# Kernel tuning notes

Measured on AMD Instinct MI355X. Metric: run time of the kernel, lower is better.

The kernel has to match this reference:

```python
import jax, jax.numpy as jnp
import numpy as np

N, B, H, L, FE = 32768, 256, 128, 4, 4
E = 262144


def setup_inputs() -> dict:
    key = jax.random.key(0)
    ks = jax.random.split(key, 16)
    def g(i, shape, scale=0.05):
        return jax.random.normal(ks[i], shape, dtype=jnp.float32) * scale
    return {
        "d": jax.random.uniform(ks[0], (E,), dtype=jnp.float32) * 5.0,
        "src": jax.random.randint(ks[1], (E,), 0, N),
        "dst": jax.random.randint(ks[2], (E,), 0, N),
        "seg": jnp.sort(jax.random.randint(ks[3], (N,), 0, B)),
        "node_emb": g(4, (H,), 1.0),
        "We": g(5, (2 * FE + 1, H)), "be": jnp.zeros((H,), jnp.float32),
        "msg_W1": g(6, (L, 3 * H, H)), "msg_b1": jnp.zeros((L, H), jnp.float32),
        "msg_W2": g(7, (L, H, H)), "msg_b2": jnp.zeros((L, H), jnp.float32),
        "soft_W": g(8, (L, H)), "soft_b": jnp.zeros((L,), jnp.float32),
        "upd_W1": g(9, (L, H, H)), "upd_b1": jnp.zeros((L, H), jnp.float32),
        "upd_W2": g(10, (L, H, H)), "upd_b2": jnp.zeros((L, H), jnp.float32),
        "out_W1": g(11, (H, H)), "out_b1": jnp.zeros((H,), jnp.float32),
        "out_W2": g(12, (H, H)), "out_b2": jnp.zeros((H,), jnp.float32),
    }


def reference(d, src, dst, seg, node_emb, We, be, msg_W1, msg_b1, msg_W2, msg_b2,
              soft_W, soft_b, upd_W1, upd_b1, upd_W2, upd_b2,
              out_W1, out_b1, out_W2, out_b2):
    silu = jax.nn.silu
    # fourier_encode_dist: [E] -> [E, 2*FE+1] = [sin(d/2^k), cos(d/2^k), d]
    scales = 2.0 ** jnp.arange(FE, dtype=d.dtype)
    x = d[:, None] / scales
    de = jnp.concatenate([jnp.sin(x), jnp.cos(x), d[:, None]], axis=-1)
    # edge_input MLP (1 layer, last_activation=SiLU) then extra F.silu in input_edge_func
    e = silu(silu(de @ We + be))                              # [E, H]
    # node_embedding broadcast to all nodes
    feat = jnp.broadcast_to(node_emb, (N, H))
    for l in range(L):
        mi = jnp.concatenate([feat[src], feat[dst], e], axis=-1)        # [E, 3H]
        m = silu(silu(mi @ msg_W1[l] + msg_b1[l]) @ msg_W2[l] + msg_b2[l])  # [E, H]
        e = e + m                                             # edge residual update
        w = jax.nn.sigmoid(m @ soft_W[l] + soft_b[l])[:, None]  # soft edge gate [E,1]
        msum = jax.ops.segment_sum(m * w, dst, num_segments=N)  # reduce to dst nodes
        upd_in = msum + feat
        feat = silu(upd_in @ upd_W1[l] + upd_b1[l]) @ upd_W2[l] + upd_b2[l] + feat
    # node-wise output network (2 layers, last activation None)
    feat = silu(feat @ out_W1 + out_b1) @ out_W2 + out_b2
    # multi-aggregator readout over graphs in batch
    s = jax.ops.segment_sum(feat, seg, num_segments=B)
    cnt = jax.ops.segment_sum(jnp.ones((N, 1), feat.dtype), seg, num_segments=B)
    mean = s / jnp.maximum(cnt, 1.0)
    mx = jax.ops.segment_max(feat, seg, num_segments=B)
    return jnp.concatenate([s, mean, mx], axis=-1)            # [B, 3H]
```

## Files before the change

kernel.cpp:

```cpp
#include <hip/hip_runtime.h>

#define NN 32768
#define NB 256
#define HD 128
#define NL 4
#define NE 262144

typedef short bf16x8 __attribute__((ext_vector_type(8)));
typedef float f32x4 __attribute__((ext_vector_type(4)));
typedef unsigned short u16;
typedef unsigned int u32;

__device__ __forceinline__ float bf2f(u16 u) {
  return __uint_as_float(((u32)u) << 16);
}
__device__ __forceinline__ u16 f2bf(float f) {
  u32 x = __float_as_uint(f);
  u32 r = x + 0x7FFFu + ((x >> 16) & 1u);
  return (u16)(r >> 16);
}
__device__ __forceinline__ u32 pk2(float a, float b) {
  return (u32)f2bf(a) | ((u32)f2bf(b) << 16);
}
__device__ __forceinline__ float siluf(float x) {
  return x * __builtin_amdgcn_rcpf(1.0f + __expf(-x));
}
__device__ __forceinline__ float sigf(float x) {
  return __builtin_amdgcn_rcpf(1.0f + __expf(-x));
}
__device__ __forceinline__ u32 ordu(float f) {
  u32 b = __float_as_uint(f);
  return (b & 0x80000000u) ? ~b : (b | 0x80000000u);
}

__device__ __forceinline__ float ldinf(const void* p, size_t i, int mode) {
  return mode ? ((const float*)p)[i] : bf2f(((const u16*)p)[i]);
}
__device__ __forceinline__ u16 ldinb(const void* p, size_t i, int mode) {
  return mode ? f2bf(((const float*)p)[i]) : ((const u16*)p)[i];
}

__global__ void k_detect(const u16* __restrict__ Weraw, int* __restrict__ flag) {
  if (threadIdx.x == 0 && blockIdx.x == 0) {
    int cnt = 0;
    for (int i = 0; i < 256; i++) {
      u16 u = Weraw[2 * i];
      u32 e = (u >> 7) & 0xFFu;
      if (e >= 112u && e <= 126u) cnt++;
    }
    *flag = (cnt >= 128) ? 0 : 1;
  }
}

__global__ __launch_bounds__(256) void k_csr_deg(const int* __restrict__ dstp,
                                                 u32* __restrict__ deg) {
  const int i = blockIdx.x * 256 + threadIdx.x;
  atomicAdd(&deg[dstp[i]], 1u);
}

__global__ __launch_bounds__(1024) void k_csr_scan(const u32* __restrict__ deg,
                                                   int* __restrict__ rowptr,
                                                   int* __restrict__ cursor) {
  __shared__ int part[1024];
  const int t = threadIdx.x;
  int loc[32];
  int s = 0;
#pragma unroll
  for (int j = 0; j < 32; j++) { loc[j] = s; s += (int)deg[t * 32 + j]; }
  part[t] = s;
  __syncthreads();
  int inc = s;
  for (int off = 1; off < 1024; off <<= 1) {
    int tmp = (t >= off) ? part[t - off] : 0;
    __syncthreads();
    part[t] += tmp;
    __syncthreads();
  }
  const int base = part[t] - inc;
#pragma unroll
  for (int j = 0; j < 32; j++) {
    rowptr[t * 32 + j] = base + loc[j];
    cursor[t * 32 + j] = base + loc[j];
  }
  if (t == 1023) rowptr[NN] = part[1023];
}

__global__ __launch_bounds__(256) void k_csr_scatter(const int* __restrict__ dstp,
                                                     int* __restrict__ cursor,
                                                     int* __restrict__ eids) {
  const int i = blockIdx.x * 256 + threadIdx.x;
  const int pos = atomicAdd(&cursor[dstp[i]], 1);
  eids[pos] = i;
}

#define PANEL 16384

template <int MT>
__device__ __forceinline__ void acc_zero(f32x4 (&acc)[MT][8]) {
#pragma unroll
  for (int mt = 0; mt < MT; mt++)
#pragma unroll
    for (int nt = 0; nt < 8; nt++) acc[mt][nt] = f32x4{0.f, 0.f, 0.f, 0.f};
}

template <int MT>
__device__ __forceinline__ void gemm_gp(const u16* __restrict__ A0,
                                        const size_t* rowoff,
                                        const u16* __restrict__ Bp,
                                        int l, int kg, f32x4 (&acc)[MT][8]) {
#pragma unroll
  for (int ks = 0; ks < 4; ks++) {
    bf16x8 a[MT];
#pragma unroll
    for (int mt = 0; mt < MT; mt++)
      a[mt] = *(const bf16x8*)&A0[rowoff[mt] + ks * 32 + kg * 8];
#pragma unroll
    for (int nt = 0; nt < 8; nt++) {
      bf16x8 b = *(const bf16x8*)&Bp[(size_t)((nt * 4 + ks) * 64 + l) * 8];
#pragma unroll
      for (int mt = 0; mt < MT; mt++)
        acc[mt][nt] = __builtin_amdgcn_mfma_f32_16x16x32_bf16(a[mt], b, acc[mt][nt], 0, 0, 0);
    }
  }
}

template <int MT>
__device__ __forceinline__ void wave_gemm_p(const short* lAw, const u16* __restrict__ Bp,
                                            int l, int c, int kg, f32x4 (&acc)[MT][8]) {
#pragma unroll
  for (int ks = 0; ks < 4; ks++) {
    bf16x8 a[MT];
#pragma unroll
    for (int mt = 0; mt < MT; mt++) {
      const int r = mt * 16 + c;
      const int k = ks * 32 + kg * 8;
      a[mt] = *(const bf16x8*)&lAw[r * HD + (k ^ ((r & 7) << 3))];
    }
#pragma unroll
    for (int nt = 0; nt < 8; nt++) {
      bf16x8 b = *(const bf16x8*)&Bp[(size_t)((nt * 4 + ks) * 64 + l) * 8];
#pragma unroll
      for (int mt = 0; mt < MT; mt++)
        acc[mt][nt] = __builtin_amdgcn_mfma_f32_16x16x32_bf16(a[mt], b, acc[mt][nt], 0, 0, 0);
    }
  }
}

template <int MT, bool SILU>
__device__ __forceinline__ void wave_pack(short* lAw, int c, int kg,
                                          f32x4 (&acc)[MT][8], const float* bias) {
#pragma unroll
  for (int mt = 0; mt < MT; mt++) {
#pragma unroll
    for (int rr = 0; rr < 4; rr++) {
      const int row = mt * 16 + kg * 4 + rr;
      u32 ou[4];
#pragma unroll
      for (int p = 0; p < 4; p++) {
        float x0 = acc[mt][2 * p][rr] + bias[2 * p];
        float x1 = acc[mt][2 * p + 1][rr] + bias[2 * p + 1];
        if (SILU) { x0 = siluf(x0); x1 = siluf(x1); }
        ou[p] = pk2(x0, x1);
      }
      ((int4*)(lAw + row * HD))[c ^ (row & 7)] =
          make_int4((int)ou[0], (int)ou[1], (int)ou[2], (int)ou[3]);
    }
  }
}

__global__ __launch_bounds__(256) void k_prep(
    const void* __restrict__ mW1, const void* __restrict__ mW2,
    const void* __restrict__ uW1, const void* __restrict__ uW2,
    const void* __restrict__ oW1, const void* __restrict__ oW2,
    const int* __restrict__ flagp,
    u16* __restrict__ Wt1, u16* __restrict__ Wt2p,
    u16* __restrict__ Wtu1, u16* __restrict__ Wtu2p,
    u16* __restrict__ Wto1, u16* __restrict__ Wto2p) {
  const int mode = *flagp;
  const int tid = blockIdx.x * blockDim.x + threadIdx.x;
  const int stride = gridDim.x * blockDim.x;
  for (int i = tid; i < NL * 3 * PANEL; i += stride) {
    const int l = i / (3 * PANEL), r = i % (3 * PANEL);
    const int chunk = r / PANEL, r2 = r % PANEL;
    const int nt = r2 / 2048, ks = (r2 % 2048) / 512;
    const int lane = (r2 % 512) / 8, j = r2 % 8;
    const int k = chunk * 128 + ks * 32 + (lane >> 4) * 8 + j;
    const int n = nt * 16 + (lane & 15);
    Wt1[i] = ldinb(mW1, ((size_t)l * 384 + k) * HD + n, mode);
  }
  for (int i = tid; i < NL * PANEL; i += stride) {
    const int l = i / PANEL, r = i % PANEL;
    const int nt = r / 2048, ks = (r % 2048) / 512;
    const int lane = (r % 512) / 8, j = r % 8;
    const int k = ks * 32 + (lane >> 4) * 8 + j;
    const int n = nt * 16 + (lane & 15);
    const int hp = ((k & 7) << 4) | (k >> 3);
    Wt2p[i] = ldinb(mW2, ((size_t)l * HD + hp) * HD + n, mode);
    Wtu1[i] = ldinb(uW1, ((size_t)l * HD + k) * HD + n, mode);
    Wtu2p[i] = ldinb(uW2, ((size_t)l * HD + hp) * HD + n, mode);
  }
  for (int i = tid; i < PANEL; i += stride) {
    const int nt = i / 2048, ks = (i % 2048) / 512;
    const int lane = (i % 512) / 8, j = i % 8;
    const int k = ks * 32 + (lane >> 4) * 8 + j;
    const int n = nt * 16 + (lane & 15);
    const int hp = ((k & 7) << 4) | (k >> 3);
    Wto1[i] = ldinb(oW1, (size_t)k * HD + n, mode);
    Wto2p[i] = ldinb(oW2, (size_t)hp * HD + n, mode);
  }
}

__global__ __launch_bounds__(256) void k_featinit(const void* __restrict__ nemb,
                                                  const int* __restrict__ flagp,
                                                  u16* __restrict__ feat) {
  const int mode = *flagp;
  const int i = blockIdx.x * 256 + threadIdx.x;
  const int g = i & 15;
  u32 ou[4];
#pragma unroll
  for (int p = 0; p < 4; p++) {
    u16 a = ldinb(nemb, g * 8 + 2 * p, mode);
    u16 b = ldinb(nemb, g * 8 + 2 * p + 1, mode);
    ou[p] = (u32)a | ((u32)b << 16);
  }
  ((int4*)feat)[i] = make_int4((int)ou[0], (int)ou[1], (int)ou[2], (int)ou[3]);
}

__global__ __launch_bounds__(256) void k_encode(const void* __restrict__ d,
                                                const void* __restrict__ We,
                                                const void* __restrict__ be,
                                                const int* __restrict__ flagp,
                                                u16* __restrict__ e) {
  const int mode = *flagp;
  __shared__ float sW[9 * HD];
  __shared__ float sb[HD];
  for (int i = threadIdx.x; i < 9 * HD; i += 256) sW[i] = ldinf(We, i, mode);
  for (int i = threadIdx.x; i < HD; i += 256) sb[i] = ldinf(be, i, mode);
  __syncthreads();
  const int eid = blockIdx.x * 256 + threadIdx.x;
  const float dv = ldinf(d, eid, mode);
  float de[9];
#pragma unroll
  for (int k = 0; k < 4; k++) {
    float x = dv * (1.0f / (float)(1 << k));
    de[k] = __sinf(x);
    de[4 + k] = __cosf(x);
  }
  de[8] = dv;
  u16* erow = e + (size_t)eid * HD;
#pragma unroll
  for (int hb = 0; hb < 16; hb++) {
    u32 ou[4];
#pragma unroll
    for (int p = 0; p < 4; p++) {
      float vv[2];
#pragma unroll
      for (int t = 0; t < 2; t++) {
        const int h = hb * 8 + 2 * p + t;
        float a = sb[h];
#pragma unroll
        for (int k = 0; k < 9; k++) a += de[k] * sW[k * HD + h];
        vv[t] = siluf(siluf(a));
      }
      ou[p] = pk2(vv[0], vv[1]);
    }
    ((int4*)erow)[hb] = make_int4((int)ou[0], (int)ou[1], (int)ou[2], (int)ou[3]);
  }
}

__global__ __launch_bounds__(64, 4) void k_edge(
    const u16* __restrict__ feat, u16* __restrict__ e,
    const int* __restrict__ src, const int* __restrict__ dstp,
    const u16* __restrict__ Wt1, const u16* __restrict__ Wt2p,
    const void* __restrict__ b1g, const void* __restrict__ b2g,
    const void* __restrict__ softW, const void* __restrict__ softb,
    const int* __restrict__ flagp, u32* __restrict__ mbuf32,
    float* __restrict__ wgbuf, int layer) {
  __shared__ __align__(16) short lM[32 * HD];
  __shared__ float swg[32];
  const int mode = *flagp;
  const int l = threadIdx.x;
  const int c = l & 15, kg = l >> 4;
  const int blk = blockIdx.x * 32;

  size_t offS[2], offD[2], offE[2];
#pragma unroll
  for (int mt = 0; mt < 2; mt++) {
    const int eidx = blk + mt * 16 + c;
    offS[mt] = (size_t)src[eidx] * HD;
    offD[mt] = (size_t)dstp[eidx] * HD;
    offE[mt] = (size_t)eidx * HD;
  }

  const u16* W1l = Wt1 + (size_t)layer * 3 * PANEL;
  const u16* W2l = Wt2p + (size_t)layer * PANEL;
  float bias1[8], bias2[8], swf[8];
#pragma unroll
  for (int nt = 0; nt < 8; nt++) {
    bias1[nt] = ldinf(b1g, layer * HD + nt * 16 + c, mode);
    bias2[nt] = ldinf(b2g, layer * HD + nt * 16 + c, mode);
    swf[nt] = ldinf(softW, (size_t)layer * HD + nt * 16 + c, mode);
  }
  const float sbv = ldinf(softb, layer, mode);

  f32x4 acc[2][8];
  acc_zero<2>(acc);
  gemm_gp<2>(feat, offS, W1l, l, kg, acc);
  gemm_gp<2>(feat, offD, W1l + PANEL, l, kg, acc);
  gemm_gp<2>(e, offE, W1l + 2 * PANEL, l, kg, acc);
  wave_pack<2, true>(lM, c, kg, acc, bias1);
  __syncthreads();

  acc_zero<2>(acc);
  wave_gemm_p<2>(lM, W2l, l, c, kg, acc);
  __syncthreads();

  float wred[2][4];
#pragma unroll
  for (int mt = 0; mt < 2; mt++) {
#pragma unroll
    for (int rr = 0; rr < 4; rr++) {
      const int row = mt * 16 + kg * 4 + rr;
      float mv[8];
      float wp = 0.f;
#pragma unroll
      for (int nt = 0; nt < 8; nt++) {
        mv[nt] = siluf(acc[mt][nt][rr] + bias2[nt]);
        wp += mv[nt] * swf[nt];
      }
      u32 ou[4];
#pragma unroll
      for (int p = 0; p < 4; p++) ou[p] = pk2(mv[2 * p], mv[2 * p + 1]);
      ((int4*)(lM + row * HD))[c ^ (row & 7)] =
          make_int4((int)ou[0], (int)ou[1], (int)ou[2], (int)ou[3]);
      wp += __shfl_xor(wp, 1);
      wp += __shfl_xor(wp, 2);
      wp += __shfl_xor(wp, 4);
      wp += __shfl_xor(wp, 8);
      wred[mt][rr] = wp;
    }
  }
#pragma unroll
  for (int mt = 0; mt < 2; mt++)
#pragma unroll
    for (int rr = 0; rr < 4; rr++)
      if (c == mt * 4 + rr) swg[mt * 16 + kg * 4 + rr] = sigf(wred[mt][rr] + sbv);
  __syncthreads();

  if (l < 32) wgbuf[blk + l] = swg[l];

  const int j1 = l >> 4;
  const int goff = l & 15;
  const bool hilane = (l >= 32);
  const int s0 = (2 * l) & 63, s1 = (2 * l + 1) & 63;
#pragma unroll 4
  for (int r = 0; r < 32; r++) {
    const int base = r * HD + ((goff ^ (r & 7)) << 3) + j1;
    const u32 m1 = (u16)lM[base];
    const u32 m2 = (u16)lM[base + 4];
    const u32 pk = m1 | (m2 << 16);
    const u32 a = (u32)__shfl((int)pk, s0);
    const u32 b = (u32)__shfl((int)pk, s1);
    const u32 lo = hilane ? (a >> 16) : (a & 0xffffu);
    const u32 hi = hilane ? (b >> 16) : (b & 0xffffu);
    mbuf32[(size_t)(blk + r) * 64 + l] = lo | (hi << 16);
    u32* erow32 = (u32*)(e + (size_t)(blk + r) * HD);
    const u32 old = erow32[l];
    erow32[l] = pk2(bf2f((u16)(old & 0xffffu)) + bf2f((u16)lo),
                    bf2f((u16)(old >> 16)) + bf2f((u16)hi));
  }
}

__global__ __launch_bounds__(256) void k_gather(
    const int* __restrict__ rowptr, const int* __restrict__ eids,
    const u32* __restrict__ mbuf32, const float* __restrict__ wgbuf,
    float* __restrict__ msum) {
  const int w = threadIdx.x >> 6;
  const int l = threadIdx.x & 63;
  const int node = blockIdx.x * 4 + w;
  const int beg = rowptr[node], end = rowptr[node + 1];
  float a0 = 0.f, a1 = 0.f;
  for (int cb = beg; cb < end; cb += 64) {
    int eL = 0;
    float wL = 0.f;
    if (cb + l < end) { eL = eids[cb + l]; wL = wgbuf[eL]; }
    const int nj = min(64, end - cb);
    for (int j = 0; j < nj; j++) {
      const int eid = __shfl(eL, j);
      const float wj = __shfl(wL, j);
      const u32 v = mbuf32[(size_t)eid * 64 + l];
      a0 += wj * bf2f((u16)(v & 0xffffu));
      a1 += wj * bf2f((u16)(v >> 16));
    }
  }
  ((float2*)(msum + (size_t)node * HD))[l] = make_float2(a0, a1);
}

__global__ __launch_bounds__(64, 2) void k_node(
    u16* __restrict__ feat, const float* __restrict__ msum,
    const u16* __restrict__ Wtu1, const u16* __restrict__ Wtu2p,
    const void* __restrict__ b1g, const void* __restrict__ b2g,
    const int* __restrict__ flagp, int layer) {
  __shared__ __align__(16) short lA[64 * HD];
  const int mode = *flagp;
  const int l = threadIdx.x;
  const int c = l & 15, kg = l >> 4;
  short* lAw = lA;
  const int blkn = blockIdx.x * 64;
  const int myrow = blkn + l;
  u16* frow = feat + (size_t)myrow * HD;
  const float* mrow = msum + (size_t)myrow * HD;
  const u16* W1l = Wtu1 + (size_t)layer * PANEL;
  const u16* W2l = Wtu2p + (size_t)layer * PANEL;
  float bias1[8], bias2[8];
#pragma unroll
  for (int nt = 0; nt < 8; nt++) {
    bias1[nt] = ldinf(b1g, layer * HD + nt * 16 + c, mode);
    bias2[nt] = ldinf(b2g, layer * HD + nt * 16 + c, mode);
  }
  {
    int4* lrow = (int4*)(lAw + l * HD);
#pragma unroll
    for (int g = 0; g < 16; g++) {
      int4 fv = ((const int4*)frow)[g];
      u32 uu[4] = {(u32)fv.x, (u32)fv.y, (u32)fv.z, (u32)fv.w};
      float4 ma = ((const float4*)mrow)[2 * g];
      float4 mb = ((const float4*)mrow)[2 * g + 1];
      float mm[8] = {ma.x, ma.y, ma.z, ma.w, mb.x, mb.y, mb.z, mb.w};
      u32 ou[4];
#pragma unroll
      for (int p = 0; p < 4; p++) {
        float a0 = bf2f((u16)(uu[p] & 0xffffu)) + mm[2 * p];
        float a1 = bf2f((u16)(uu[p] >> 16)) + mm[2 * p + 1];
        ou[p] = pk2(a0, a1);
      }
      lrow[g ^ (l & 7)] = make_int4((int)ou[0], (int)ou[1], (int)ou[2], (int)ou[3]);
    }
  }
  __syncthreads();
  f32x4 acc[4][8];
  acc_zero<4>(acc);
  wave_gemm_p<4>(lAw, W1l, l, c, kg, acc);
  __syncthreads();
  wave_pack<4, true>(lAw, c, kg, acc, bias1);
  __syncthreads();
  acc_zero<4>(acc);
  wave_gemm_p<4>(lAw, W2l, l, c, kg, acc);
  __syncthreads();
  wave_pack<4, false>(lAw, c, kg, acc, bias2);
  __syncthreads();

  const int j1 = l >> 4;
  const int goff = l & 15;
  const bool hilane = (l >= 32);
  const int s0 = (2 * l) & 63, s1 = (2 * l + 1) & 63;
#pragma unroll 4
  for (int r = 0; r < 64; r++) {
    const int base = r * HD + ((goff ^ (r & 7)) << 3) + j1;
    const u32 m1 = (u16)lAw[base];
    const u32 m2 = (u16)lAw[base + 4];
    const u32 pk = m1 | (m2 << 16);
    const u32 a = (u32)__shfl((int)pk, s0);
    const u32 b = (u32)__shfl((int)pk, s1);
    const u32 lo = hilane ? (a >> 16) : (a & 0xffffu);
    const u32 hi = hilane ? (b >> 16) : (b & 0xffffu);
    u32* frow32 = (u32*)(feat + (size_t)(blkn + r) * HD);
    const u32 old = frow32[l];
    frow32[l] = pk2(bf2f((u16)(old & 0xffffu)) + bf2f((u16)lo),
                    bf2f((u16)(old >> 16)) + bf2f((u16)hi));
  }
}

__global__ __launch_bounds__(64, 2) void k_out(
    const u16* __restrict__ feat, const int* __restrict__ seg,
    const u16* __restrict__ Wto1, const u16* __restrict__ Wto2p,
    const void* __restrict__ ob1, const void* __restrict__ ob2,
    const int* __restrict__ flagp,
    float* __restrict__ sacc, u32* __restrict__ mxacc, float* __restrict__ cnt) {
  __shared__ __align__(16) short lA[64 * HD];
  __shared__ int sseg[64];
  const int mode = *flagp;
  const int l = threadIdx.x;
  const int c = l & 15, kg = l >> 4;
  short* lAw = lA;
  const int myrow = blockIdx.x * 64 + l;
  const u16* frow = feat + (size_t)myrow * HD;
  float bias1[8], bias2[8];
#pragma unroll
  for (int nt = 0; nt < 8; nt++) {
    bias1[nt] = ldinf(ob1, nt * 16 + c, mode);
    bias2[nt] = ldinf(ob2, nt * 16 + c, mode);
  }
  {
    int4* lrow = (int4*)(lAw + l * HD);
#pragma unroll
    for (int g = 0; g < 16; g++) lrow[g ^ (l & 7)] = ((const int4*)frow)[g];
  }
  sseg[l] = seg[myrow];
  __syncthreads();
  f32x4 acc[4][8];
  acc_zero<4>(acc);
  wave_gemm_p<4>(lAw, Wto1, l, c, kg, acc);
  __syncthreads();
  wave_pack<4, true>(lAw, c, kg, acc, bias1);
  __syncthreads();
  acc_zero<4>(acc);
  wave_gemm_p<4>(lAw, Wto2p, l, c, kg, acc);
  __syncthreads();
  wave_pack<4, false>(lAw, c, kg, acc, bias2);
  __syncthreads();

  const int j1 = l >> 4;
  const int goff = l & 15;
  const bool uniform = (sseg[0] == sseg[63]);
  if (uniform) {
    const int g = sseg[0];
    float s1 = 0.f, s2 = 0.f, x1 = -3.402823e38f, x2 = -3.402823e38f;
#pragma unroll 4
    for (int r = 0; r < 64; r++) {
      const int base = r * HD + ((goff ^ (r & 7)) << 3) + j1;
      const float v1 = bf2f((u16)lAw[base]);
      const float v2 = bf2f((u16)lAw[base + 4]);
      s1 += v1; s2 += v2;
      x1 = fmaxf(x1, v1); x2 = fmaxf(x2, v2);
    }
    atomicAdd(&sacc[(size_t)g * HD + l], s1);
    atomicAdd(&sacc[(size_t)g * HD + l + 64], s2);
    atomicMax(&mxacc[(size_t)g * HD + l], ordu(x1));
    atomicMax(&mxacc[(size_t)g * HD + l + 64], ordu(x2));
    if (l == 0) atomicAdd(&cnt[g], 64.0f);
  } else {
    atomicAdd(&cnt[sseg[l]], 1.0f);
#pragma unroll 4
    for (int r = 0; r < 64; r++) {
      const int base = r * HD + ((goff ^ (r & 7)) << 3) + j1;
      const float v1 = bf2f((u16)lAw[base]);
      const float v2 = bf2f((u16)lAw[base + 4]);
      const int g = sseg[r];
      atomicAdd(&sacc[(size_t)g * HD + l], v1);
      atomicAdd(&sacc[(size_t)g * HD + l + 64], v2);
      atomicMax(&mxacc[(size_t)g * HD + l], ordu(v1));
      atomicMax(&mxacc[(size_t)g * HD + l + 64], ordu(v2));
    }
  }
}

__global__ __launch_bounds__(256) void k_final(const float* __restrict__ sacc,
                                               const u32* __restrict__ mxacc,
                                               const float* __restrict__ cnt,
                                               const int* __restrict__ flagp,
                                               void* __restrict__ out) {
  const int mode = *flagp;
  const int i = blockIdx.x * 256 + threadIdx.x;
  const int b = i / 384, j = i % 384;
  float v;
  if (j < HD) v = sacc[b * HD + j];
  else if (j < 2 * HD) v = sacc[b * HD + (j - HD)] / fmaxf(cnt[b], 1.0f);
  else {
    u32 u = mxacc[b * HD + (j - 2 * HD)];
    u32 bits = (u >> 31) ? (u ^ 0x80000000u) : ~u;
    v = __uint_as_float(bits);
  }
  if (mode) ((float*)out)[i] = v;
  else ((u16*)out)[i] = f2bf(v);
}

extern "C" void kernel_launch(void* const* d_in, const int* in_sizes, int n_in,
                              void* d_out, int out_size, void* d_ws, size_t ws_size,
                              hipStream_t stream) {
  const void* d_d = d_in[0];
  const int* src = (const int*)d_in[1];
  const int* dst = (const int*)d_in[2];
  const int* seg = (const int*)d_in[3];
  const void* nemb = d_in[4];
  const void* We = d_in[5];
  const void* be = d_in[6];
  const void* mW1 = d_in[7];
  const void* mb1 = d_in[8];
  const void* mW2 = d_in[9];
  const void* mb2 = d_in[10];
  const void* sW = d_in[11];
  const void* sb = d_in[12];
  const void* uW1 = d_in[13];
  const void* ub1 = d_in[14];
  const void* uW2 = d_in[15];
  const void* ub2 = d_in[16];
  const void* oW1 = d_in[17];
  const void* ob1 = d_in[18];
  const void* oW2 = d_in[19];
  const void* ob2 = d_in[20];

  char* ws = (char*)d_ws;
  const size_t OFF_E = 0;
  const size_t OFF_MBUF = OFF_E + (size_t)NE * HD * 2;
  const size_t OFF_WG = OFF_MBUF + (size_t)NE * HD * 2;
  const size_t OFF_MSUM = OFF_WG + (size_t)NE * 4;
  const size_t OFF_FEAT = OFF_MSUM + (size_t)NN * HD * 4;
  const size_t OFF_SACC = OFF_FEAT + (size_t)NN * HD * 2;
  const size_t OFF_MX = OFF_SACC + (size_t)NB * HD * 4;
  const size_t OFF_CNT = OFF_MX + (size_t)NB * HD * 4;
  const size_t OFF_DEG = OFF_CNT + 1024;
  const size_t OFF_ROWPTR = OFF_DEG + (size_t)NN * 4;
  const size_t OFF_CURSOR = OFF_ROWPTR + (size_t)(NN + 2) * 4;
  const size_t OFF_EIDS = OFF_CURSOR + (size_t)NN * 4;
  const size_t OFF_WT1 = OFF_EIDS + (size_t)NE * 4;
  const size_t OFF_WT2P = OFF_WT1 + (size_t)NL * 3 * PANEL * 2;
  const size_t OFF_WTU1 = OFF_WT2P + (size_t)NL * PANEL * 2;
  const size_t OFF_WTU2P = OFF_WTU1 + (size_t)NL * PANEL * 2;
  const size_t OFF_WTO1 = OFF_WTU2P + (size_t)NL * PANEL * 2;
  const size_t OFF_WTO2P = OFF_WTO1 + (size_t)PANEL * 2;
  const size_t OFF_FLAG = OFF_WTO2P + (size_t)PANEL * 2;

  u16* e = (u16*)(ws + OFF_E);
  u32* mbuf32 = (u32*)(ws + OFF_MBUF);
  float* wgbuf = (float*)(ws + OFF_WG);
  float* msum = (float*)(ws + OFF_MSUM);
  u16* feat = (u16*)(ws + OFF_FEAT);
  float* sacc = (float*)(ws + OFF_SACC);
  u32* mx = (u32*)(ws + OFF_MX);
  float* cnt = (float*)(ws + OFF_CNT);
  u32* deg = (u32*)(ws + OFF_DEG);
  int* rowptr = (int*)(ws + OFF_ROWPTR);
  int* cursor = (int*)(ws + OFF_CURSOR);
  int* eids = (int*)(ws + OFF_EIDS);
  u16* Wt1 = (u16*)(ws + OFF_WT1);
  u16* Wt2p = (u16*)(ws + OFF_WT2P);
  u16* Wtu1 = (u16*)(ws + OFF_WTU1);
  u16* Wtu2p = (u16*)(ws + OFF_WTU2P);
  u16* Wto1 = (u16*)(ws + OFF_WTO1);
  u16* Wto2p = (u16*)(ws + OFF_WTO2P);
  int* flag = (int*)(ws + OFF_FLAG);

  hipMemsetAsync(ws + OFF_SACC, 0,
                 (size_t)NB * HD * 4 * 2 + 1024 + (size_t)NN * 4, stream);

  k_detect<<<1, 64, 0, stream>>>((const u16*)We, flag);
  k_prep<<<256, 256, 0, stream>>>(mW1, mW2, uW1, uW2, oW1, oW2, flag,
                                  Wt1, Wt2p, Wtu1, Wtu2p, Wto1, Wto2p);
  k_featinit<<<(NN * HD / 8) / 256, 256, 0, stream>>>(nemb, flag, feat);
  k_encode<<<NE / 256, 256, 0, stream>>>(d_d, We, be, flag, e);

  k_csr_deg<<<NE / 256, 256, 0, stream>>>(dst, deg);
  k_csr_scan<<<1, 1024, 0, stream>>>(deg, rowptr, cursor);
  k_csr_scatter<<<NE / 256, 256, 0, stream>>>(dst, cursor, eids);

  for (int l = 0; l < NL; l++) {
    k_edge<<<NE / 32, 64, 0, stream>>>(feat, e, src, dst, Wt1, Wt2p,
                                       mb1, mb2, sW, sb, flag, mbuf32, wgbuf, l);
    k_gather<<<NN / 4, 256, 0, stream>>>(rowptr, eids, mbuf32, wgbuf, msum);
    k_node<<<NN / 64, 64, 0, stream>>>(feat, msum, Wtu1, Wtu2p, ub1, ub2, flag, l);
  }
  k_out<<<NN / 64, 64, 0, stream>>>(feat, seg, Wto1, Wto2p, ob1, ob2, flag, sacc, mx, cnt);
  k_final<<<(NB * 384) / 256, 256, 0, stream>>>(sacc, mx, cnt, flag, d_out);
}
```

Baseline: 822.9 us.

## Store activations in a permuted hidden-dim layout to drop shuffle-based unpacking

Switches the stored hidden-dimension order of edge features, node features and messages to a permuted layout, where logical index h sits at physical position (h%16)*8 + h/16. The permutation is folded into the pre-transposed weight panels, the encoder, the feature init and the final output un-permute. As a result the epilogues of the edge, node and output kernels can read one packed 32-bit word from shared memory per row. This replaces two 16-bit LDS reads, two cross-lane shuffles and select logic. The cost is a consistent permutation that every kernel must honour, so any mismatch would silently corrupt results.

```diff
diff --git a/kernel.cpp b/kernel.cpp
--- a/kernel.cpp
+++ b/kernel.cpp
@@ -51,6 +51,7 @@
     *flag = (cnt >= 128) ? 0 : 1;
   }
 }
+
 
 __global__ __launch_bounds__(256) void k_csr_deg(const int* __restrict__ dstp,
                                                  u32* __restrict__ deg) {
@@ -184,29 +185,30 @@
     const int chunk = r / PANEL, r2 = r % PANEL;
     const int nt = r2 / 2048, ks = (r2 % 2048) / 512;
     const int lane = (r2 % 512) / 8, j = r2 % 8;
-    const int k = chunk * 128 + ks * 32 + (lane >> 4) * 8 + j;
+    const int s = ks * 32 + (lane >> 4) * 8 + j;
+    const int klog = ((s & 7) << 4) | (s >> 3);
     const int n = nt * 16 + (lane & 15);
-    Wt1[i] = ldinb(mW1, ((size_t)l * 384 + k) * HD + n, mode);
+    Wt1[i] = ldinb(mW1, ((size_t)l * 384 + chunk * 128 + klog) * HD + n, mode);
   }
   for (int i = tid; i < NL * PANEL; i += stride) {
     const int l = i / PANEL, r = i % PANEL;
     const int nt = r / 2048, ks = (r % 2048) / 512;
     const int lane = (r % 512) / 8, j = r % 8;
-    const int k = ks * 32 + (lane >> 4) * 8 + j;
+    const int s = ks * 32 + (lane >> 4) * 8 + j;
+    const int klog = ((s & 7) << 4) | (s >> 3);
     const int n = nt * 16 + (lane & 15);
-    const int hp = ((k & 7) << 4) | (k >> 3);
-    Wt2p[i] = ldinb(mW2, ((size_t)l * HD + hp) * HD + n, mode);
-    Wtu1[i] = ldinb(uW1, ((size_t)l * HD + k) * HD + n, mode);
-    Wtu2p[i] = ldinb(uW2, ((size_t)l * HD + hp) * HD + n, mode);
+    Wt2p[i] = ldinb(mW2, ((size_t)l * HD + klog) * HD + n, mode);
+    Wtu1[i] = ldinb(uW1, ((size_t)l * HD + klog) * HD + n, mode);
+    Wtu2p[i] = ldinb(uW2, ((size_t)l * HD + klog) * HD + n, mode);
   }
   for (int i = tid; i < PANEL; i += stride) {
     const int nt = i / 2048, ks = (i % 2048) / 512;
     const int lane = (i % 512) / 8, j = i % 8;
-    const int k = ks * 32 + (lane >> 4) * 8 + j;
+    const int s = ks * 32 + (lane >> 4) * 8 + j;
+    const int klog = ((s & 7) << 4) | (s >> 3);
     const int n = nt * 16 + (lane & 15);
-    const int hp = ((k & 7) << 4) | (k >> 3);
-    Wto1[i] = ldinb(oW1, (size_t)k * HD + n, mode);
-    Wto2p[i] = ldinb(oW2, (size_t)hp * HD + n, mode);
+    Wto1[i] = ldinb(oW1, (size_t)klog * HD + n, mode);
+    Wto2p[i] = ldinb(oW2, (size_t)klog * HD + n, mode);
   }
 }
 
@@ -219,8 +221,8 @@
   u32 ou[4];
 #pragma unroll
   for (int p = 0; p < 4; p++) {
-    u16 a = ldinb(nemb, g * 8 + 2 * p, mode);
-    u16 b = ldinb(nemb, g * 8 + 2 * p + 1, mode);
+    u16 a = ldinb(nemb, (2 * p) * 16 + g, mode);
+    u16 b = ldinb(nemb, (2 * p + 1) * 16 + g, mode);
     ou[p] = (u32)a | ((u32)b << 16);
   }
   ((int4*)feat)[i] = make_int4((int)ou[0], (int)ou[1], (int)ou[2], (int)ou[3]);
@@ -249,14 +251,14 @@
   de[8] = dv;
   u16* erow = e + (size_t)eid * HD;
 #pragma unroll
-  for (int hb = 0; hb < 16; hb++) {
+  for (int g = 0; g < 16; g++) {
     u32 ou[4];
 #pragma unroll
     for (int p = 0; p < 4; p++) {
       float vv[2];
 #pragma unroll
       for (int t = 0; t < 2; t++) {
-        const int h = hb * 8 + 2 * p + t;
+        const int h = (2 * p + t) * 16 + g;
         float a = sb[h];
 #pragma unroll
         for (int k = 0; k < 9; k++) a += de[k] * sW[k * HD + h];
@@ -264,7 +266,7 @@
       }
       ou[p] = pk2(vv[0], vv[1]);
     }
-    ((int4*)erow)[hb] = make_int4((int)ou[0], (int)ou[1], (int)ou[2], (int)ou[3]);
+    ((int4*)erow)[g] = make_int4((int)ou[0], (int)ou[1], (int)ou[2], (int)ou[3]);
   }
 }
 
@@ -349,25 +351,16 @@
 
   if (l < 32) wgbuf[blk + l] = swg[l];
 
-  const int j1 = l >> 4;
-  const int goff = l & 15;
-  const bool hilane = (l >= 32);
-  const int s0 = (2 * l) & 63, s1 = (2 * l + 1) & 63;
+  const int gL = l >> 2;
+  const int eoff = (l & 3) * 2;
 #pragma unroll 4
   for (int r = 0; r < 32; r++) {
-    const int base = r * HD + ((goff ^ (r & 7)) << 3) + j1;
-    const u32 m1 = (u16)lM[base];
-    const u32 m2 = (u16)lM[base + 4];
-    const u32 pk = m1 | (m2 << 16);
-    const u32 a = (u32)__shfl((int)pk, s0);
-    const u32 b = (u32)__shfl((int)pk, s1);
-    const u32 lo = hilane ? (a >> 16) : (a & 0xffffu);
-    const u32 hi = hilane ? (b >> 16) : (b & 0xffffu);
-    mbuf32[(size_t)(blk + r) * 64 + l] = lo | (hi << 16);
+    const u32 mv = *(const u32*)&lM[r * HD + ((gL ^ (r & 7)) << 3) + eoff];
+    mbuf32[(size_t)(blk + r) * 64 + l] = mv;
     u32* erow32 = (u32*)(e + (size_t)(blk + r) * HD);
     const u32 old = erow32[l];
-    erow32[l] = pk2(bf2f((u16)(old & 0xffffu)) + bf2f((u16)lo),
-                    bf2f((u16)(old >> 16)) + bf2f((u16)hi));
+    erow32[l] = pk2(bf2f((u16)(old & 0xffffu)) + bf2f((u16)(mv & 0xffffu)),
+                    bf2f((u16)(old >> 16)) + bf2f((u16)(mv >> 16)));
   }
 }
 
@@ -450,24 +443,15 @@
   wave_pack<4, false>(lAw, c, kg, acc, bias2);
   __syncthreads();
 
-  const int j1 = l >> 4;
-  const int goff = l & 15;
-  const bool hilane = (l >= 32);
-  const int s0 = (2 * l) & 63, s1 = (2 * l + 1) & 63;
+  const int gL = l >> 2;
+  const int eoff = (l & 3) * 2;
 #pragma unroll 4
   for (int r = 0; r < 64; r++) {
-    const int base = r * HD + ((goff ^ (r & 7)) << 3) + j1;
-    const u32 m1 = (u16)lAw[base];
-    const u32 m2 = (u16)lAw[base + 4];
-    const u32 pk = m1 | (m2 << 16);
-    const u32 a = (u32)__shfl((int)pk, s0);
-    const u32 b = (u32)__shfl((int)pk, s1);
-    const u32 lo = hilane ? (a >> 16) : (a & 0xffffu);
-    const u32 hi = hilane ? (b >> 16) : (b & 0xffffu);
+    const u32 mv = *(const u32*)&lAw[r * HD + ((gL ^ (r & 7)) << 3) + eoff];
     u32* frow32 = (u32*)(feat + (size_t)(blkn + r) * HD);
     const u32 old = frow32[l];
-    frow32[l] = pk2(bf2f((u16)(old & 0xffffu)) + bf2f((u16)lo),
-                    bf2f((u16)(old >> 16)) + bf2f((u16)hi));
+    frow32[l] = pk2(bf2f((u16)(old & 0xffffu)) + bf2f((u16)(mv & 0xffffu)),
+                    bf2f((u16)(old >> 16)) + bf2f((u16)(mv >> 16)));
   }
 }
 
@@ -510,37 +494,37 @@
   wave_pack<4, false>(lAw, c, kg, acc, bias2);
   __syncthreads();
 
-  const int j1 = l >> 4;
-  const int goff = l & 15;
+  const int gL = l >> 2;
+  const int eoff = (l & 3) * 2;
   const bool uniform = (sseg[0] == sseg[63]);
   if (uniform) {
     const int g = sseg[0];
     float s1 = 0.f, s2 = 0.f, x1 = -3.402823e38f, x2 = -3.402823e38f;
 #pragma unroll 4
     for (int r = 0; r < 64; r++) {
-      const int base = r * HD + ((goff ^ (r & 7)) << 3) + j1;
-      const float v1 = bf2f((u16)lAw[base]);
-      const float v2 = bf2f((u16)lAw[base + 4]);
+      const u32 mv = *(const u32*)&lAw[r * HD + ((gL ^ (r & 7)) << 3) + eoff];
+      const float v1 = bf2f((u16)(mv & 0xffffu));
+      const float v2 = bf2f((u16)(mv >> 16));
       s1 += v1; s2 += v2;
       x1 = fmaxf(x1, v1); x2 = fmaxf(x2, v2);
     }
-    atomicAdd(&sacc[(size_t)g * HD + l], s1);
-    atomicAdd(&sacc[(size_t)g * HD + l + 64], s2);
-    atomicMax(&mxacc[(size_t)g * HD + l], ordu(x1));
-    atomicMax(&mxacc[(size_t)g * HD + l + 64], ordu(x2));
+    atomicAdd(&sacc[(size_t)g * HD + 2 * l], s1);
+    atomicAdd(&sacc[(size_t)g * HD + 2 * l + 1], s2);
+    atomicMax(&mxacc[(size_t)g * HD + 2 * l], ordu(x1));
+    atomicMax(&mxacc[(size_t)g * HD + 2 * l + 1], ordu(x2));
     if (l == 0) atomicAdd(&cnt[g], 64.0f);
   } else {
     atomicAdd(&cnt[sseg[l]], 1.0f);
 #pragma unroll 4
     for (int r = 0; r < 64; r++) {
-      const int base = r * HD + ((goff ^ (r & 7)) << 3) + j1;
-      const float v1 = bf2f((u16)lAw[base]);
-      const float v2 = bf2f((u16)lAw[base + 4]);
+      const u32 mv = *(const u32*)&lAw[r * HD + ((gL ^ (r & 7)) << 3) + eoff];
+      const float v1 = bf2f((u16)(mv & 0xffffu));
+      const float v2 = bf2f((u16)(mv >> 16));
       const int g = sseg[r];
-      atomicAdd(&sacc[(size_t)g * HD + l], v1);
-      atomicAdd(&sacc[(size_t)g * HD + l + 64], v2);
-      atomicMax(&mxacc[(size_t)g * HD + l], ordu(v1));
-      atomicMax(&mxacc[(size_t)g * HD + l + 64], ordu(v2));
+      atomicAdd(&sacc[(size_t)g * HD + 2 * l], v1);
+      atomicAdd(&sacc[(size_t)g * HD + 2 * l + 1], v2);
+      atomicMax(&mxacc[(size_t)g * HD + 2 * l], ordu(v1));
+      atomicMax(&mxacc[(size_t)g * HD + 2 * l + 1], ordu(v2));
     }
   }
 }
@@ -554,10 +538,17 @@
   const int i = blockIdx.x * 256 + threadIdx.x;
   const int b = i / 384, j = i % 384;
   float v;
-  if (j < HD) v = sacc[b * HD + j];
-  else if (j < 2 * HD) v = sacc[b * HD + (j - HD)] / fmaxf(cnt[b], 1.0f);
-  else {
-    u32 u = mxacc[b * HD + (j - 2 * HD)];
+  if (j < HD) {
+    const int p = ((j & 15) << 3) | (j >> 4);
+    v = sacc[b * HD + p];
+  } else if (j < 2 * HD) {
+    const int t = j - HD;
+    const int p = ((t & 15) << 3) | (t >> 4);
+    v = sacc[b * HD + p] / fmaxf(cnt[b], 1.0f);
+  } else {
+    const int t = j - 2 * HD;
+    const int p = ((t & 15) << 3) | (t >> 4);
+    u32 u = mxacc[b * HD + p];
     u32 bits = (u >> 31) ? (u ^ 0x80000000u) : ~u;
     v = __uint_as_float(bits);
   }
```

Result: slower. 857.2 us (+4.2%).
